# Performance work log

Hardware: AMD Instinct MI355X
Metric: run time of the kernel (lower is better)

Reference implementation:

```python
import jax, jax.numpy as jnp
import numpy as np
from jax import lax

X_SIZE, Z_SIZE, H, GC, PD = 256, 64, 64, 16, 2
B, K, T = 256, 16, 50
LOG_SIG_MIN, LOG_SIG_MAX, LOG_P_MAX = -10.0, 10.0, 50.0
ZX = X_SIZE + Z_SIZE
LSTM_IN = ZX + PD


def setup_inputs() -> dict:
    key = jax.random.key(0)
    ks = jax.random.split(key, 24)
    s = lambda fan_in: 1.0 / np.sqrt(fan_in)
    u = lambda k, shape, sc: jax.random.uniform(k, shape, jnp.float32, -sc, sc)
    inp = {
        'x': jax.random.normal(ks[0], (B, X_SIZE), jnp.float32),
        'z_stacked': jax.random.normal(ks[1], (K, B, Z_SIZE), jnp.float32),
        'input_seqs': jax.random.normal(ks[2], (B, 8, 2, 2, 6), jnp.float32),
        'pred_seqs': jax.random.normal(ks[3], (B, T, 2, 2, 6), jnp.float32),
        # initial_h / initial_c linears: ZX -> H
        'Wh0': u(ks[4], (H, ZX), s(ZX)), 'bh0': u(ks[5], (H,), s(ZX)),
        'Wc0': u(ks[6], (H, ZX), s(ZX)), 'bc0': u(ks[7], (H,), s(ZX)),
        # LSTMCell: gates order i,f,g,o
        'Wih': u(ks[8], (4 * H, LSTM_IN), s(H)), 'Whh': u(ks[9], (4 * H, H), s(H)),
        'bih': u(ks[10], (4 * H,), s(H)), 'bhh': u(ks[11], (4 * H,), s(H)),
        # GMM parameter heads: H -> GC / GC*PD
        'Wpi': u(ks[12], (GC, H), s(H)), 'bpi': u(ks[13], (GC,), s(H)),
        'Wmu': u(ks[14], (GC * PD, H), s(H)), 'bmu': u(ks[15], (GC * PD,), s(H)),
        'Wls': u(ks[16], (GC * PD, H), s(H)), 'bls': u(ks[17], (GC * PD,), s(H)),
        'Wcorr': u(ks[18], (GC, H), s(H)), 'bcorr': u(ks[19], (GC,), s(H)),
        'n_z_samples': K,
    }
    return inp


def _gmm2d_log_prob(log_pis, mus, log_sigmas, corrs, value):
    # log_pis/corrs: [K,B,T,GC]; mus/log_sigmas: [K,B,T,GC*PD]; value: [B,T,PD]
    ls = jnp.clip(log_sigmas, LOG_SIG_MIN, LOG_SIG_MAX).reshape(K, B, T, GC, PD)
    mu = mus.reshape(K, B, T, GC, PD)
    dx = value[None, :, :, None, :] - mu                      # [K,B,T,GC,PD]
    zscore = dx * jnp.exp(-ls)                                # dx / sigma
    one_m_rho2 = 1.0 - corrs ** 2
    quad = (zscore[..., 0] ** 2 + zscore[..., 1] ** 2
            - 2.0 * corrs * zscore[..., 0] * zscore[..., 1])
    comp = (-jnp.log(2.0 * jnp.pi) - ls.sum(-1)
            - 0.5 * jnp.log(one_m_rho2) - 0.5 * quad / one_m_rho2)
    log_pi_n = jax.nn.log_softmax(log_pis, axis=-1)
    log_p_t = jax.nn.logsumexp(log_pi_n + comp, axis=-1)      # [K,B,T]
    return jnp.minimum(log_p_t, LOG_P_MAX)


def reference(x, z_stacked, input_seqs, pred_seqs,
              Wh0, bh0, Wc0, bc0, Wih, Whh, bih, bhh,
              Wpi, bpi, Wmu, bmu, Wls, bls, Wcorr, bcorr, n_z_samples):
    tgt_future = pred_seqs[:, :, 1, 1, 2:4]                   # [B,T,2]
    tgt_present = input_seqs[:, -1, 1, 1, 2:4]                # [B,2]
    z = z_stacked.reshape(-1, z_stacked.shape[-1])            # [K*B, z]
    zx = jnp.concatenate([z, jnp.tile(x, (n_z_samples, 1))], axis=1)  # [N, ZX]
    N = zx.shape[0]
    h0 = zx @ Wh0.T + bh0
    c0 = zx @ Wc0.T + bc0
    decode_inputs = jnp.concatenate([tgt_present[:, None, :], tgt_future[:, :T - 1, :]], axis=1)  # [B,T,2]
    inputs = jnp.concatenate([
        jnp.broadcast_to(zx[:, None, :], (N, T, ZX)),
        jnp.tile(decode_inputs, (n_z_samples, 1, 1))], axis=2)  # [N,T,ZX+2]

    def step(carry, xt):
        h, c = carry
        gates = xt @ Wih.T + bih + h @ Whh.T + bhh
        i, f, g, o = jnp.split(gates, 4, axis=-1)
        c = jax.nn.sigmoid(f) * c + jax.nn.sigmoid(i) * jnp.tanh(g)
        h = jax.nn.sigmoid(o) * jnp.tanh(c)
        return (h, c), h

    _, hs = lax.scan(step, (h0, c0), jnp.swapaxes(inputs, 0, 1))  # [T,N,H]
    hs = jnp.swapaxes(hs, 0, 1)                                   # [N,T,H]

    log_pis = (hs @ Wpi.T + bpi).reshape(K, B, T, GC)
    mus = (hs @ Wmu.T + bmu).reshape(K, B, T, GC * PD)
    log_sigmas = (hs @ Wls.T + bls).reshape(K, B, T, GC * PD)
    corrs = jnp.tanh(hs @ Wcorr.T + bcorr).reshape(K, B, T, GC)

    log_p_yt_xz = _gmm2d_log_prob(log_pis, mus, log_sigmas, corrs, tgt_future)
    return log_p_yt_xz.sum(axis=2)                                # [K,B]
```

## Files before the change

### kernel.cpp

```cpp
#include <hip/hip_runtime.h>


#define T_ 50
typedef __attribute__((ext_vector_type(8))) short short8;
typedef __attribute__((ext_vector_type(4))) float f32x4;
#define MFMA(a,b,c) __builtin_amdgcn_mfma_f32_16x16x32_bf16(a,b,c,0,0,0)

#define HOUT_B 0u
#define WF_B   26214400u
#define WIH_S 0
#define WH0_S 320
#define WC0_S 400
#define WHH_S 480
#define PRJ_S 512

__device__ __forceinline__ float sigf(float x)  { return 1.0f / (1.0f + __expf(-x)); }
__device__ __forceinline__ float tanh_(float x) { return 1.0f - 2.0f / (__expf(2.0f * x) + 1.0f); }

__device__ __forceinline__ void splitf(float f, unsigned short& hi, unsigned short& lo) {
    unsigned b = __float_as_uint(f);
    hi = (unsigned short)(b >> 16);
    float fh = __uint_as_float(b & 0xffff0000u);
    lo = (unsigned short)(__float_as_uint(f - fh) >> 16);
}
__device__ __forceinline__ void pack8(const float* p, short8& hi, short8& lo) {
    #pragma unroll
    for (int e = 0; e < 8; ++e) {
        unsigned short h, l;
        splitf(p[e], h, l);
        hi[e] = (short)h; lo[e] = (short)l;
    }
}
__device__ __forceinline__ unsigned short bf16rn(float f) {
    unsigned b = __float_as_uint(f);
    unsigned r = b + 0x7fffu + ((b >> 16) & 1u);
    return (unsigned short)(r >> 16);
}
__device__ __forceinline__ void pack8rn(const float* p, short8& hi) {
    #pragma unroll
    for (int e = 0; e < 8; ++e) hi[e] = (short)bf16rn(p[e]);
}

__global__ void pack_kernel(const float* __restrict__ Wih, const float* __restrict__ Whh,
                            const float* __restrict__ Wh0, const float* __restrict__ Wc0,
                            const float* __restrict__ Wpi, const float* __restrict__ Wmu,
                            const float* __restrict__ Wls, const float* __restrict__ Wcorr,
                            short8* __restrict__ WF)
{
    int id = blockIdx.x * 256 + threadIdx.x;
    if (id >= 18176) return;
    if (id < 10240) {
        int ks = id >> 10, rem = id & 1023;
        int q = rem >> 8, w = (rem >> 6) & 3, l = rem & 63;
        int g = l >> 4, c = l & 15;
        const float* src = Wih + (q*64 + w*16 + c)*322 + ks*32 + g*8;
        short8 hi, lo; pack8(src, hi, lo);
        WF[(WIH_S + ((ks*4 + q)*2 + 0)*4 + w)*64 + l] = hi;
        WF[(WIH_S + ((ks*4 + q)*2 + 1)*4 + w)*64 + l] = lo;
    } else if (id < 12800) {
        int t2 = id - 10240;
        int ks = t2 >> 8, w = (t2 >> 6) & 3, l = t2 & 63;
        int g = l >> 4, c = l & 15;
        const float* src = Wh0 + (w*16 + c)*320 + ks*32 + g*8;
        short8 hi, lo; pack8(src, hi, lo);
        WF[(WH0_S + (ks*2 + 0)*4 + w)*64 + l] = hi;
        WF[(WH0_S + (ks*2 + 1)*4 + w)*64 + l] = lo;
    } else if (id < 15360) {
        int t2 = id - 12800;
        int ks = t2 >> 8, w = (t2 >> 6) & 3, l = t2 & 63;
        int g = l >> 4, c = l & 15;
        const float* src = Wc0 + (w*16 + c)*320 + ks*32 + g*8;
        short8 hi, lo; pack8(src, hi, lo);
        WF[(WC0_S + (ks*2 + 0)*4 + w)*64 + l] = hi;
        WF[(WC0_S + (ks*2 + 1)*4 + w)*64 + l] = lo;
    } else if (id < 17408) {
        int t3 = id - 15360;
        int slot = t3 >> 6, l = t3 & 63;
        int g = l >> 4, c = l & 15;
        int tile = slot >> 1, ks = slot & 1;
        int q = tile >> 2, wt = tile & 3;
        short8 hi; pack8rn(Whh + (q*64 + 16*wt + c)*64 + ks*32 + g*8, hi);
        WF[(WHH_S + slot)*64 + l] = hi;
    } else {
        int t4 = id - 17408;
        int r = t4 >> 6, l = t4 & 63;
        int g = l >> 4, c = l & 15;
        int pt = r >> 1, ks = r & 1;
        int r3 = pt*16 + c;
        const float* p;
        if      (r3 < 16) p = Wpi   + r3*64;
        else if (r3 < 48) p = Wmu   + (r3-16)*64;
        else if (r3 < 80) p = Wls   + (r3-48)*64;
        else              p = Wcorr + (r3-80)*64;
        short8 hi, lo; pack8(p + ks*32 + g*8, hi, lo);
        WF[(PRJ_S + ((pt*2 + ks)*2 + 0))*64 + l] = hi;
        WF[(PRJ_S + ((pt*2 + ks)*2 + 1))*64 + l] = lo;
    }
}

__launch_bounds__(256, 2)
__global__ void lstm_kernel(
    const float* __restrict__ x,        const float* __restrict__ z,
    const float* __restrict__ inp_seqs, const float* __restrict__ pred_seqs,
    const float* __restrict__ Wih,      const float* __restrict__ bh0,
    const float* __restrict__ bc0,      const float* __restrict__ bih,
    const float* __restrict__ bhh,
    unsigned short* __restrict__ Hout,  const short8* __restrict__ WF)
{
    __shared__ __align__(16) float smem[6336];
    float* ZXL = smem;
    float* DQ  = smem;
    unsigned short* HF0h = (unsigned short*)(smem + 5184);
    unsigned short* HF0l = (unsigned short*)(smem + 5472);
    unsigned short* HF1h = (unsigned short*)(smem + 5760);
    unsigned short* HF1l = (unsigned short*)(smem + 6048);

    const int j = threadIdx.x;
    const int w = j >> 6, l = j & 63, g = l >> 4, c = l & 15;
    const int U = 16*w + c;
    const int blk = blockIdx.x, nb = blk*16;

    for (int e = j; e < 16*320; e += 256) {
        int s = e / 320, k = e - s*320;
        int n = nb + s, b = n & 255;
        ZXL[s*324 + k] = (k < 64) ? z[n*64 + k] : x[b*256 + (k - 64)];
    }
    __syncthreads();

    f32x4 gcA[4], h0a, c0a;
    {
        #pragma unroll
        for (int q = 0; q < 4; ++q) {
            int ga = q*64 + U;
            float b_ = bih[ga] + bhh[ga];
            gcA[q] = (f32x4){b_, b_, b_, b_};
        }
        float bh_ = bh0[U], bc_ = bc0[U];
        h0a = (f32x4){bh_, bh_, bh_, bh_};
        c0a = (f32x4){bc_, bc_, bc_, bc_};
    }
    for (int ks = 0; ks < 10; ++ks) {
        short8 ah, al;
        pack8(&ZXL[c*324 + ks*32 + g*8], ah, al);
        #pragma unroll
        for (int q = 0; q < 4; ++q) {
            short8 Bh = WF[(WIH_S + ((ks*4 + q)*2 + 0)*4 + w)*64 + l];
            short8 Bl = WF[(WIH_S + ((ks*4 + q)*2 + 1)*4 + w)*64 + l];
            gcA[q] = MFMA(ah, Bh, gcA[q]);
            gcA[q] = MFMA(ah, Bl, gcA[q]);
            gcA[q] = MFMA(al, Bh, gcA[q]);
        }
        {
            short8 Bh = WF[(WH0_S + (ks*2 + 0)*4 + w)*64 + l];
            short8 Bl = WF[(WH0_S + (ks*2 + 1)*4 + w)*64 + l];
            h0a = MFMA(ah, Bh, h0a); h0a = MFMA(ah, Bl, h0a); h0a = MFMA(al, Bh, h0a);
        }
        {
            short8 Bh = WF[(WC0_S + (ks*2 + 0)*4 + w)*64 + l];
            short8 Bl = WF[(WC0_S + (ks*2 + 1)*4 + w)*64 + l];
            c0a = MFMA(ah, Bh, c0a); c0a = MFMA(ah, Bl, c0a); c0a = MFMA(al, Bh, c0a);
        }
    }
    float cst[4];
    #pragma unroll
    for (int r = 0; r < 4; ++r) {
        cst[r] = c0a[r];
        unsigned short hh, ll; splitf(h0a[r], hh, ll);
        HF0h[(4*g + r)*72 + U] = hh;
        HF0l[(4*g + r)*72 + U] = ll;
    }
    float wd0[4], wd1[4];
    #pragma unroll
    for (int q = 0; q < 4; ++q) {
        int ga = q*64 + U;
        wd0[q] = Wih[ga*322 + 320];
        wd1[q] = Wih[ga*322 + 321];
    }
    short8 WB[4][2];
    #pragma unroll
    for (int q = 0; q < 4; ++q)
        #pragma unroll
        for (int ks = 0; ks < 2; ++ks)
            WB[q][ks] = WF[(WHH_S + (q*4 + w)*2 + ks)*64 + l];
    __syncthreads();

    for (int e = j; e < T_*32; e += 256) {
        int t = e >> 5, rem = e & 31, s = rem >> 1, comp = rem & 1;
        int b = (nb + s) & 255;
        DQ[e] = (t == 0) ? inp_seqs[b*192 + 188 + comp]
                         : pred_seqs[b*1200 + (t-1)*24 + 20 + comp];
    }
    __syncthreads();

    for (int t = 0; t < T_; ++t) {
        const unsigned short* Hh = (t & 1) ? HF1h : HF0h;
        const unsigned short* Hl = (t & 1) ? HF1l : HF0l;
        unsigned short* Nh = (t & 1) ? HF0h : HF1h;
        unsigned short* Nl = (t & 1) ? HF0l : HF1l;

        short8 ah0 = *reinterpret_cast<const short8*>(Hh + c*72 +      g*8);
        short8 al0 = *reinterpret_cast<const short8*>(Hl + c*72 +      g*8);
        short8 ah1 = *reinterpret_cast<const short8*>(Hh + c*72 + 32 + g*8);
        short8 al1 = *reinterpret_cast<const short8*>(Hl + c*72 + 32 + g*8);
        f32x4 dA = *reinterpret_cast<const f32x4*>(DQ + t*32 + 8*g);
        f32x4 dB = *reinterpret_cast<const f32x4*>(DQ + t*32 + 8*g + 4);

        f32x4 aq[4];
        #pragma unroll
        for (int q = 0; q < 4; ++q) {
            f32x4 a;
            a[0] = gcA[q][0] + dA[0]*wd0[q] + dA[1]*wd1[q];
            a[1] = gcA[q][1] + dA[2]*wd0[q] + dA[3]*wd1[q];
            a[2] = gcA[q][2] + dB[0]*wd0[q] + dB[1]*wd1[q];
            a[3] = gcA[q][3] + dB[2]*wd0[q] + dB[3]*wd1[q];
            a = MFMA(ah0, WB[q][0], a);
            a = MFMA(al0, WB[q][0], a);
            a = MFMA(ah1, WB[q][1], a);
            a = MFMA(al1, WB[q][1], a);
            aq[q] = a;
        }
        #pragma unroll
        for (int r = 0; r < 4; ++r) {
            float cc = sigf(aq[1][r])*cst[r] + sigf(aq[0][r])*tanh_(aq[2][r]);
            cst[r] = cc;
            float hv = sigf(aq[3][r])*tanh_(cc);
            unsigned short hh, ll; splitf(hv, hh, ll);
            Nh[(4*g + r)*72 + U] = hh;
            Nl[(4*g + r)*72 + U] = ll;
            Hout[(size_t)(t*4096 + nb + 4*g + r)*64 + U] = hh;
        }
        asm volatile("s_waitcnt lgkmcnt(0)" ::: "memory");
        __builtin_amdgcn_s_barrier();
        asm volatile("" ::: "memory");
    }
}

__launch_bounds__(256, 3)
__global__ void head_kernel(const float* __restrict__ pred_seqs,
                            const float* __restrict__ bpi, const float* __restrict__ bmu,
                            const float* __restrict__ bls, const float* __restrict__ bcorr,
                            const unsigned short* __restrict__ Hin,
                            const short8* __restrict__ WF,
                            float* __restrict__ out)
{
    __shared__ __align__(16) float PL[4][1600];
    const int j = threadIdx.x;
    const int w = j >> 6;
    const int l = j & 63;
    const int g = l >> 4;
    const int c = l & 15;
    const int blk = blockIdx.x;
    const int set = blk >> 2, chunk = blk & 3;
    const int t0 = (chunk*25) >> 1, t1 = ((chunk+1)*25) >> 1;

    float bias[6];
    #pragma unroll
    for (int pt = 0; pt < 6; ++pt) {
        int r3 = pt*16 + c;
        bias[pt] = (r3 < 16) ? bpi[r3] : (r3 < 48) ? bmu[r3-16]
                 : (r3 < 80) ? bls[r3-48] : bcorr[r3-80];
    }

    const int s = l >> 2, q4 = l & 3;
    const int n_s = set*16 + s, b_s = n_s & 255;
    float* PLw = &PL[w][0];
    float sum_local = 0.0f;

    for (int t = t0 + w; t < t1; t += 4) {
        const unsigned short* hp = Hin + (size_t)(t*4096 + set*16 + c)*64;
        short8 ah0 = *reinterpret_cast<const short8*>(hp + g*8);
        short8 ah1 = *reinterpret_cast<const short8*>(hp + 32 + g*8);
        #pragma unroll
        for (int pt = 0; pt < 6; ++pt) {
            short8 B00 = WF[(PRJ_S + ((pt*2 + 0)*2 + 0))*64 + l];
            short8 B01 = WF[(PRJ_S + ((pt*2 + 0)*2 + 1))*64 + l];
            short8 B10 = WF[(PRJ_S + ((pt*2 + 1)*2 + 0))*64 + l];
            short8 B11 = WF[(PRJ_S + ((pt*2 + 1)*2 + 1))*64 + l];
            f32x4 p = (f32x4){bias[pt], bias[pt], bias[pt], bias[pt]};
            p = MFMA(ah0, B00, p);
            p = MFMA(ah0, B01, p);
            p = MFMA(ah1, B10, p);
            p = MFMA(ah1, B11, p);
            #pragma unroll
            for (int r = 0; r < 4; ++r) PLw[(4*g + r)*100 + pt*16 + c] = p[r];
        }
        asm volatile("s_waitcnt lgkmcnt(0)" ::: "memory");
        __builtin_amdgcn_sched_barrier(0);

        float2 tv = *reinterpret_cast<const float2*>(pred_seqs + b_s*1200 + t*24 + 20);
        float a[4], m = -1e30f, Ppi = 0.0f;
        #pragma unroll
        for (int i = 0; i < 4; ++i) {
            int cq = q4*4 + i;
            float pi = PLw[s*100 + cq];
            float2 mu = *reinterpret_cast<const float2*>(PLw + s*100 + 16 + 2*cq);
            float2 ls = *reinterpret_cast<const float2*>(PLw + s*100 + 48 + 2*cq);
            float co = PLw[s*100 + 80 + cq];
            float l0 = fminf(fmaxf(ls.x, -10.0f), 10.0f);
            float l1 = fminf(fmaxf(ls.y, -10.0f), 10.0f);
            float z0 = (tv.x - mu.x) * __expf(-l0);
            float z1 = (tv.y - mu.y) * __expf(-l1);
            float ct = tanh_(co);
            float omr = 1.0f - ct*ct;
            float quad = z0*z0 + z1*z1 - 2.0f*ct*z0*z1;
            float comp = -1.8378770664093453f - (l0 + l1) - 0.5f*__logf(omr) - 0.5f*quad/omr;
            a[i] = pi + comp;
            m = fmaxf(m, a[i]);
            Ppi += __expf(pi);
        }
        m = fmaxf(m, __shfl_xor(m, 1));
        m = fmaxf(m, __shfl_xor(m, 2));
        float E = __expf(a[0]-m) + __expf(a[1]-m) + __expf(a[2]-m) + __expf(a[3]-m);
        E   += __shfl_xor(E, 1);   E   += __shfl_xor(E, 2);
        Ppi += __shfl_xor(Ppi, 1); Ppi += __shfl_xor(Ppi, 2);
        float logp = m + __logf(E) - __logf(Ppi);
        sum_local += fminf(logp, 50.0f);
    }
    if (q4 == 0) atomicAdd(out + n_s, sum_local);
}

extern "C" void kernel_launch(void* const* d_in, const int* in_sizes, int n_in,
                              void* d_out, int out_size, void* d_ws, size_t ws_size,
                              hipStream_t stream) {
    const float* x     = (const float*)d_in[0];
    const float* z     = (const float*)d_in[1];
    const float* iseq  = (const float*)d_in[2];
    const float* pseq  = (const float*)d_in[3];
    const float* Wh0   = (const float*)d_in[4];
    const float* bh0   = (const float*)d_in[5];
    const float* Wc0   = (const float*)d_in[6];
    const float* bc0   = (const float*)d_in[7];
    const float* Wih   = (const float*)d_in[8];
    const float* Whh   = (const float*)d_in[9];
    const float* bih   = (const float*)d_in[10];
    const float* bhh   = (const float*)d_in[11];
    const float* Wpi   = (const float*)d_in[12];
    const float* bpi   = (const float*)d_in[13];
    const float* Wmu   = (const float*)d_in[14];
    const float* bmu   = (const float*)d_in[15];
    const float* Wls   = (const float*)d_in[16];
    const float* bls   = (const float*)d_in[17];
    const float* Wcorr = (const float*)d_in[18];
    const float* bcorr = (const float*)d_in[19];
    float* out = (float*)d_out;

    char* ws = (char*)d_ws;
    unsigned short* Hout = (unsigned short*)(ws + HOUT_B);
    short8* WF = (short8*)(ws + WF_B);

    pack_kernel<<<71, 256, 0, stream>>>(Wih, Whh, Wh0, Wc0, Wpi, Wmu, Wls, Wcorr, WF);
    hipMemsetAsync(d_out, 0, 4096 * sizeof(float), stream);
    lstm_kernel<<<256, 256, 0, stream>>>(x, z, iseq, pseq, Wih, bh0, bc0, bih, bhh,
                                         Hout, (const short8*)WF);
    head_kernel<<<1024, 256, 0, stream>>>(pseq, bpi, bmu, bls, bcorr,
                                          (const unsigned short*)Hout,
                                          (const short8*)WF, out);
}
```

Before: 110.7 us.

## Split LSTM across 1024 blocks of 4 sequences, single-bf16 head projection

The LSTM kernel now handles 4 sequences per block instead of 16 and launches 1024 blocks with a higher occupancy bound. Only row 0 of each 4-row MFMA tile is used, with the other rows zero-padded, so the 50-step serial recurrence is spread over more CUs. The head projection weights drop the hi/lo split and use a single rounded bf16 word, halving the head MFMAs and Hout is written with round-to-nearest. In exchange, three quarters of each MFMA in the recurrence is wasted, the zx input projection is recomputed with padding, and the head loses some precision.

```diff
diff --git a/kernel.cpp b/kernel.cpp
--- a/kernel.cpp
+++ b/kernel.cpp
@@ -13,6 +13,8 @@
 #define WC0_S 400
 #define WHH_S 480
 #define PRJ_S 512
+
+#define HFS 76
 
 __device__ __forceinline__ float sigf(float x)  { return 1.0f / (1.0f + __expf(-x)); }
 __device__ __forceinline__ float tanh_(float x) { return 1.0f - 2.0f / (__expf(2.0f * x) + 1.0f); }
@@ -92,13 +94,12 @@
         else if (r3 < 48) p = Wmu   + (r3-16)*64;
         else if (r3 < 80) p = Wls   + (r3-48)*64;
         else              p = Wcorr + (r3-80)*64;
-        short8 hi, lo; pack8(p + ks*32 + g*8, hi, lo);
-        WF[(PRJ_S + ((pt*2 + ks)*2 + 0))*64 + l] = hi;
-        WF[(PRJ_S + ((pt*2 + ks)*2 + 1))*64 + l] = lo;
-    }
-}
-
-__launch_bounds__(256, 2)
+        short8 hi; pack8rn(p + ks*32 + g*8, hi);
+        WF[(PRJ_S + r)*64 + l] = hi;
+    }
+}
+
+__launch_bounds__(256, 4)
 __global__ void lstm_kernel(
     const float* __restrict__ x,        const float* __restrict__ z,
     const float* __restrict__ inp_seqs, const float* __restrict__ pred_seqs,
@@ -107,34 +108,39 @@
     const float* __restrict__ bhh,
     unsigned short* __restrict__ Hout,  const short8* __restrict__ WF)
 {
-    __shared__ __align__(16) float smem[6336];
-    float* ZXL = smem;
-    float* DQ  = smem;
-    unsigned short* HF0h = (unsigned short*)(smem + 5184);
-    unsigned short* HF0l = (unsigned short*)(smem + 5472);
-    unsigned short* HF1h = (unsigned short*)(smem + 5760);
-    unsigned short* HF1l = (unsigned short*)(smem + 6048);
+    __shared__ __align__(16) float ZXL[16*324];
+    __shared__ __align__(16) float DQ[T_*8];
+    __shared__ __align__(16) unsigned short HP[4][16*HFS];
 
     const int j = threadIdx.x;
     const int w = j >> 6, l = j & 63, g = l >> 4, c = l & 15;
     const int U = 16*w + c;
-    const int blk = blockIdx.x, nb = blk*16;
-
-    for (int e = j; e < 16*320; e += 256) {
+    const int blk = blockIdx.x, nb = blk*4;
+
+    for (int e = j; e < 16*324; e += 256) ZXL[e] = 0.0f;
+    for (int e = j; e < 4*16*HFS; e += 256) (&HP[0][0])[e] = 0;
+    __syncthreads();
+    for (int e = j; e < 4*320; e += 256) {
         int s = e / 320, k = e - s*320;
         int n = nb + s, b = n & 255;
-        ZXL[s*324 + k] = (k < 64) ? z[n*64 + k] : x[b*256 + (k - 64)];
+        ZXL[(4*s)*324 + k] = (k < 64) ? z[n*64 + k] : x[b*256 + (k - 64)];
+    }
+    for (int e = j; e < T_*8; e += 256) {
+        int t = e >> 3, rem = e & 7, s = rem >> 1, comp = rem & 1;
+        int b = (nb + s) & 255;
+        DQ[e] = (t == 0) ? inp_seqs[b*192 + 188 + comp]
+                         : pred_seqs[b*1200 + (t-1)*24 + 20 + comp];
     }
     __syncthreads();
 
     f32x4 gcA[4], h0a, c0a;
+    #pragma unroll
+    for (int q = 0; q < 4; ++q) {
+        int ga = q*64 + U;
+        float b_ = bih[ga] + bhh[ga];
+        gcA[q] = (f32x4){b_, b_, b_, b_};
+    }
     {
-        #pragma unroll
-        for (int q = 0; q < 4; ++q) {
-            int ga = q*64 + U;
-            float b_ = bih[ga] + bhh[ga];
-            gcA[q] = (f32x4){b_, b_, b_, b_};
-        }
         float bh_ = bh0[U], bc_ = bc0[U];
         h0a = (f32x4){bh_, bh_, bh_, bh_};
         c0a = (f32x4){bc_, bc_, bc_, bc_};
@@ -161,13 +167,14 @@
             c0a = MFMA(ah, Bh, c0a); c0a = MFMA(ah, Bl, c0a); c0a = MFMA(al, Bh, c0a);
         }
     }
-    float cst[4];
-    #pragma unroll
-    for (int r = 0; r < 4; ++r) {
-        cst[r] = c0a[r];
-        unsigned short hh, ll; splitf(h0a[r], hh, ll);
-        HF0h[(4*g + r)*72 + U] = hh;
-        HF0l[(4*g + r)*72 + U] = ll;
+    float gcs[4];
+    #pragma unroll
+    for (int q = 0; q < 4; ++q) gcs[q] = gcA[q][0];
+    float cst = c0a[0];
+    {
+        unsigned short hh, ll; splitf(h0a[0], hh, ll);
+        HP[0][(4*g)*HFS + U] = hh;
+        HP[1][(4*g)*HFS + U] = ll;
     }
     float wd0[4], wd1[4];
     #pragma unroll
@@ -182,53 +189,43 @@
         #pragma unroll
         for (int ks = 0; ks < 2; ++ks)
             WB[q][ks] = WF[(WHH_S + (q*4 + w)*2 + ks)*64 + l];
-    __syncthreads();
-
-    for (int e = j; e < T_*32; e += 256) {
-        int t = e >> 5, rem = e & 31, s = rem >> 1, comp = rem & 1;
-        int b = (nb + s) & 255;
-        DQ[e] = (t == 0) ? inp_seqs[b*192 + 188 + comp]
-                         : pred_seqs[b*1200 + (t-1)*24 + 20 + comp];
-    }
-    __syncthreads();
+
+    asm volatile("s_waitcnt lgkmcnt(0)" ::: "memory");
+    __builtin_amdgcn_s_barrier();
+    asm volatile("" ::: "memory");
 
     for (int t = 0; t < T_; ++t) {
-        const unsigned short* Hh = (t & 1) ? HF1h : HF0h;
-        const unsigned short* Hl = (t & 1) ? HF1l : HF0l;
-        unsigned short* Nh = (t & 1) ? HF0h : HF1h;
-        unsigned short* Nl = (t & 1) ? HF0l : HF1l;
-
-        short8 ah0 = *reinterpret_cast<const short8*>(Hh + c*72 +      g*8);
-        short8 al0 = *reinterpret_cast<const short8*>(Hl + c*72 +      g*8);
-        short8 ah1 = *reinterpret_cast<const short8*>(Hh + c*72 + 32 + g*8);
-        short8 al1 = *reinterpret_cast<const short8*>(Hl + c*72 + 32 + g*8);
-        f32x4 dA = *reinterpret_cast<const f32x4*>(DQ + t*32 + 8*g);
-        f32x4 dB = *reinterpret_cast<const f32x4*>(DQ + t*32 + 8*g + 4);
+        const unsigned short* Hh = HP[2*(t & 1)];
+        const unsigned short* Hl = HP[2*(t & 1) + 1];
+        unsigned short* Nh = HP[2*((t + 1) & 1)];
+        unsigned short* Nl = HP[2*((t + 1) & 1) + 1];
+
+        short8 ah0 = *reinterpret_cast<const short8*>(Hh + c*HFS +      g*8);
+        short8 al0 = *reinterpret_cast<const short8*>(Hl + c*HFS +      g*8);
+        short8 ah1 = *reinterpret_cast<const short8*>(Hh + c*HFS + 32 + g*8);
+        short8 al1 = *reinterpret_cast<const short8*>(Hl + c*HFS + 32 + g*8);
+        float dx = DQ[t*8 + g*2], dy = DQ[t*8 + g*2 + 1];
 
         f32x4 aq[4];
         #pragma unroll
         for (int q = 0; q < 4; ++q) {
             f32x4 a;
-            a[0] = gcA[q][0] + dA[0]*wd0[q] + dA[1]*wd1[q];
-            a[1] = gcA[q][1] + dA[2]*wd0[q] + dA[3]*wd1[q];
-            a[2] = gcA[q][2] + dB[0]*wd0[q] + dB[1]*wd1[q];
-            a[3] = gcA[q][3] + dB[2]*wd0[q] + dB[3]*wd1[q];
+            a[0] = gcs[q] + dx*wd0[q] + dy*wd1[q];
+            a[1] = 0.0f; a[2] = 0.0f; a[3] = 0.0f;
             a = MFMA(ah0, WB[q][0], a);
             a = MFMA(al0, WB[q][0], a);
             a = MFMA(ah1, WB[q][1], a);
             a = MFMA(al1, WB[q][1], a);
             aq[q] = a;
         }
-        #pragma unroll
-        for (int r = 0; r < 4; ++r) {
-            float cc = sigf(aq[1][r])*cst[r] + sigf(aq[0][r])*tanh_(aq[2][r]);
-            cst[r] = cc;
-            float hv = sigf(aq[3][r])*tanh_(cc);
-            unsigned short hh, ll; splitf(hv, hh, ll);
-            Nh[(4*g + r)*72 + U] = hh;
-            Nl[(4*g + r)*72 + U] = ll;
-            Hout[(size_t)(t*4096 + nb + 4*g + r)*64 + U] = hh;
-        }
+        float cc = sigf(aq[1][0])*cst + sigf(aq[0][0])*tanh_(aq[2][0]);
+        cst = cc;
+        float hv = sigf(aq[3][0])*tanh_(cc);
+        unsigned short hh, ll; splitf(hv, hh, ll);
+        Nh[(4*g)*HFS + U] = hh;
+        Nl[(4*g)*HFS + U] = ll;
+        Hout[(size_t)(t*4096 + nb + g)*64 + U] = bf16rn(hv);
+
         asm volatile("s_waitcnt lgkmcnt(0)" ::: "memory");
         __builtin_amdgcn_s_barrier();
         asm volatile("" ::: "memory");
@@ -272,15 +269,11 @@
         short8 ah1 = *reinterpret_cast<const short8*>(hp + 32 + g*8);
         #pragma unroll
         for (int pt = 0; pt < 6; ++pt) {
-            short8 B00 = WF[(PRJ_S + ((pt*2 + 0)*2 + 0))*64 + l];
-            short8 B01 = WF[(PRJ_S + ((pt*2 + 0)*2 + 1))*64 + l];
-            short8 B10 = WF[(PRJ_S + ((pt*2 + 1)*2 + 0))*64 + l];
-            short8 B11 = WF[(PRJ_S + ((pt*2 + 1)*2 + 1))*64 + l];
+            short8 B0 = WF[(PRJ_S + pt*2 + 0)*64 + l];
+            short8 B1 = WF[(PRJ_S + pt*2 + 1)*64 + l];
             f32x4 p = (f32x4){bias[pt], bias[pt], bias[pt], bias[pt]};
-            p = MFMA(ah0, B00, p);
-            p = MFMA(ah0, B01, p);
-            p = MFMA(ah1, B10, p);
-            p = MFMA(ah1, B11, p);
+            p = MFMA(ah0, B0, p);
+            p = MFMA(ah1, B1, p);
             #pragma unroll
             for (int r = 0; r < 4; ++r) PLw[(4*g + r)*100 + pt*16 + c] = p[r];
         }
@@ -350,8 +343,8 @@
 
     pack_kernel<<<71, 256, 0, stream>>>(Wih, Whh, Wh0, Wc0, Wpi, Wmu, Wls, Wcorr, WF);
     hipMemsetAsync(d_out, 0, 4096 * sizeof(float), stream);
-    lstm_kernel<<<256, 256, 0, stream>>>(x, z, iseq, pseq, Wih, bh0, bc0, bih, bhh,
-                                         Hout, (const short8*)WF);
+    lstm_kernel<<<1024, 256, 0, stream>>>(x, z, iseq, pseq, Wih, bh0, bc0, bih, bhh,
+                                          Hout, (const short8*)WF);
     head_kernel<<<1024, 256, 0, stream>>>(pseq, bpi, bmu, bls, bcorr,
                                           (const unsigned short*)Hout,
                                           (const short8*)WF, out);
```

Measured after the change: 146.0 us. 1.32x slower.
